# Kernel tuning notes

Hardware: AMD Instinct MI355X
Metric: run time of the kernel (lower is better)

Reference implementation:

```python
import jax, jax.numpy as jnp
import numpy as np

B, T, ND, SD, H = 4096, 256, 16, 8, 64
IN = SD + ND  # LSTM input dim


def setup_inputs() -> dict:
    key = jax.random.key(0)
    ks = jax.random.split(key, 20)
    def w(k, shape):
        fan_in = shape[0]
        return jax.random.normal(k, shape, jnp.float32) / np.sqrt(fan_in)
    return {
        "noise": jax.random.normal(ks[0], (B, T - 1, ND), jnp.float32),
        "eps": jax.random.normal(ks[1], (B, T - 1, SD), jnp.float32),
        "Wx": w(ks[2], (IN, 4 * H)),
        "Wh": w(ks[3], (H, 4 * H)),
        "b": jnp.zeros((4 * H,), jnp.float32),
        "Wm1": w(ks[4], (H, H)), "bm1": jnp.zeros((H,), jnp.float32),
        "Wm2": w(ks[5], (H, H)), "bm2": jnp.zeros((H,), jnp.float32),
        "Wm3": w(ks[6], (H, SD)), "bm3": jnp.zeros((SD,), jnp.float32),
        "Wv1": w(ks[7], (H, H)), "bv1": jnp.zeros((H,), jnp.float32),
        "Wv2": w(ks[8], (H, H)), "bv2": jnp.zeros((H,), jnp.float32),
        "Wv3": w(ks[9], (H, SD)), "bv3": jnp.zeros((SD,), jnp.float32),
    }


def reference(noise, eps, Wx, Wh, b, Wm1, bm1, Wm2, bm2, Wm3, bm3,
              Wv1, bv1, Wv2, bv2, Wv3, bv3):
    Bn = noise.shape[0]
    Hn = Wh.shape[0]
    Dn = Wm3.shape[1]

    def mlp(h, W1, b1, W2, b2, W3, b3):
        a = jax.nn.relu(h @ W1 + b1)
        a = jax.nn.relu(a @ W2 + b2)
        return a @ W3 + b3

    def step(carry, inp_t):
        x, h, c = carry
        n_t, e_t = inp_t
        # Keras LSTM: gates ordered i, f, g(cell), o
        z = jnp.concatenate([x, n_t], axis=-1) @ Wx + h @ Wh + b  # [B, 4H]
        i, f, g, o = jnp.split(z, 4, axis=-1)
        c = jax.nn.sigmoid(f) * c + jax.nn.sigmoid(i) * jnp.tanh(g)
        h = jax.nn.sigmoid(o) * jnp.tanh(c)
        mu = mlp(h, Wm1, bm1, Wm2, bm2, Wm3, bm3)
        std = jnp.exp(0.5 * mlp(h, Wv1, bv1, Wv2, bv2, Wv3, bv3))
        x = mu + std * e_t  # reparameterized Normal(mu, std).sample()
        return (x, h, c), x

    x0 = jnp.zeros((Bn, Dn), noise.dtype)  # log_series=True -> zeros
    h0 = jnp.zeros((Bn, Hn), noise.dtype)
    c0 = jnp.zeros((Bn, Hn), noise.dtype)
    noise_t = jnp.swapaxes(noise, 0, 1)  # [T-1, B, ND]
    eps_t = jnp.swapaxes(eps, 0, 1)      # [T-1, B, SD]
    _, xs = jax.lax.scan(step, (x0, h0, c0), (noise_t, eps_t))
    seq = jnp.concatenate([x0[:, None, :], jnp.swapaxes(xs, 0, 1)], axis=1)  # [B, T, SD]
    return jnp.cumsum(seq, axis=1)
```

## Files before the change

kernel.cpp:

```cpp
#include <hip/hip_runtime.h>

typedef _Float16 half8 __attribute__((ext_vector_type(8)));
typedef _Float16 half4 __attribute__((ext_vector_type(4)));
typedef float f32x4 __attribute__((ext_vector_type(4)));

#define TSTEPS 255
#define R 16
#define BLK 512
#define XSH 104
#define ZS 260
#define ASH 72

__device__ __forceinline__ float frcp(float x) { return __builtin_amdgcn_rcpf(x); }

__device__ __forceinline__ f32x4 mfma16(half8 a, half8 b, f32x4 c) {
  return __builtin_amdgcn_mfma_f32_16x16x32_f16(a, b, c, 0, 0, 0);
}

__global__ __launch_bounds__(BLK)
void genlstm_kernel(const float* __restrict__ noise,
                    const float* __restrict__ eps,
                    const float* __restrict__ Wx,
                    const float* __restrict__ Wh,
                    const float* __restrict__ bg,
                    const float* __restrict__ Wm1, const float* __restrict__ bm1,
                    const float* __restrict__ Wm2, const float* __restrict__ bm2,
                    const float* __restrict__ Wm3, const float* __restrict__ bm3,
                    const float* __restrict__ Wv1, const float* __restrict__ bv1,
                    const float* __restrict__ Wv2, const float* __restrict__ bv2,
                    const float* __restrict__ Wv3, const float* __restrict__ bv3,
                    float* __restrict__ out)
{
  __shared__ __align__(16) _Float16 xh[R][XSH];
  __shared__ __align__(16) _Float16 xl[R][XSH];
  __shared__ __align__(16) float    z2[R][ZS];
  __shared__ __align__(16) _Float16 a1h[2][R][ASH];
  __shared__ __align__(16) _Float16 a1l[2][R][ASH];
  __shared__ __align__(16) _Float16 a2h[2][R][ASH];
  __shared__ __align__(16) _Float16 a2l[2][R][ASH];
  __shared__ __align__(16) float    mulv[2][R][12];

  const int tid  = threadIdx.x;
  const int w    = tid >> 6;
  const int l    = tid & 63;
  const int lrow = l & 15;
  const int lq   = l >> 4;
  const long rowbase = (long)blockIdx.x * R;

  half8 gBhi[2][3], gBlo[2][3];
  #pragma unroll
  for (int t = 0; t < 2; ++t)
    #pragma unroll
    for (int kt = 0; kt < 3; ++kt)
      #pragma unroll
      for (int j = 0; j < 8; ++j) {
        int k  = 32 * kt + 8 * lq + j;
        int jc = 32 * w + 16 * t + lrow;
        int n  = 64 * (jc & 3) + (jc >> 2);
        float v = 0.f;
        if (k < 64) v = Wh[k * 256 + n];
        else if (k < 88) v = Wx[(k - 64) * 256 + n];
        _Float16 h = (_Float16)v;
        gBhi[t][kt][j] = h;
        gBlo[t][kt][j] = (_Float16)(v - (float)h);
      }

  const int chain = w >> 2;
  const int nt = w & 3;
  const float* W1 = chain ? Wv1 : Wm1;
  const float* W2 = chain ? Wv2 : Wm2;
  half8 B1hi[2], B1lo[2], B2hi[2], B2lo[2];
  #pragma unroll
  for (int kt = 0; kt < 2; ++kt)
    #pragma unroll
    for (int j = 0; j < 8; ++j) {
      int k = 32 * kt + 8 * lq + j;
      int n = 16 * nt + lrow;
      float v1 = W1[k * 64 + n];
      _Float16 h1 = (_Float16)v1;
      B1hi[kt][j] = h1; B1lo[kt][j] = (_Float16)(v1 - (float)h1);
      float v2 = W2[k * 64 + n];
      _Float16 h2 = (_Float16)v2;
      B2hi[kt][j] = h2; B2lo[kt][j] = (_Float16)(v2 - (float)h2);
    }

  half8 B3hi[2], B3lo[2];
  if (w < 2) {
    const float* W3 = w ? Wv3 : Wm3;
    #pragma unroll
    for (int kt = 0; kt < 2; ++kt)
      #pragma unroll
      for (int j = 0; j < 8; ++j) {
        int k = 32 * kt + 8 * lq + j;
        float v = (lrow < 8) ? W3[k * 8 + lrow] : 0.f;
        _Float16 h = (_Float16)v;
        B3hi[kt][j] = h;
        B3lo[kt][j] = (_Float16)(v - (float)h);
      }
  }

  const float bias1 = (chain ? bv1 : bm1)[16 * nt + lrow];
  const float bias2 = (chain ? bv2 : bm2)[16 * nt + lrow];
  float bias3 = 0.f;
  if (w < 2 && lrow < 8) bias3 = (w ? bv3 : bm3)[lrow];

  const float4 bgq = {bg[l], bg[64 + l], bg[128 + l], bg[192 + l]};

  float cst0 = 0.f, cst1 = 0.f;
  const int r5 = tid >> 3, d5 = tid & 7;
  float cum = 0.f;

  half8 hHi[2], hLo[2];
  #pragma unroll
  for (int kt = 0; kt < 2; ++kt)
    #pragma unroll
    for (int j = 0; j < 8; ++j) { hHi[kt][j] = (_Float16)0; hLo[kt][j] = (_Float16)0; }

  for (int i = tid; i < R * XSH; i += BLK) {
    (&xh[0][0])[i] = (_Float16)0;
    (&xl[0][0])[i] = (_Float16)0;
  }
  if (tid < 128) out[((rowbase + r5) * 256) * 8 + d5] = 0.f;
  __syncthreads();

  float4 nz = {0.f, 0.f, 0.f, 0.f};
  if (tid < 64) {
    int r = tid >> 2, j4 = (tid & 3) * 4;
    float4 n0 = *(const float4*)&noise[((rowbase + r) * TSTEPS) * 16 + j4];
    float tmp[4] = {n0.x, n0.y, n0.z, n0.w};
    half4 nh, nl;
    #pragma unroll
    for (int j = 0; j < 4; ++j) {
      _Float16 h = (_Float16)tmp[j];
      nh[j] = h; nl[j] = (_Float16)(tmp[j] - (float)h);
    }
    *(half4*)&xh[r][72 + j4] = nh;
    *(half4*)&xl[r][72 + j4] = nl;
    nz = *(const float4*)&noise[((rowbase + r) * TSTEPS + 1) * 16 + j4];
  }
  float ev = 0.f;
  if (tid < 128) ev = eps[((rowbase + r5) * TSTEPS) * 8 + d5];
  __syncthreads();

  for (int ts = 0; ts < TSTEPS; ++ts) {
    half8 Xhi = *(const half8*)&xh[lrow][64 + 8 * lq];
    half8 Xlo = *(const half8*)&xl[lrow][64 + 8 * lq];

    f32x4 accz0 = {0.f, 0.f, 0.f, 0.f};
    f32x4 accz1 = {0.f, 0.f, 0.f, 0.f};
    accz0 = mfma16(hHi[0], gBhi[0][0], accz0);
    accz1 = mfma16(hHi[0], gBhi[1][0], accz1);
    accz0 = mfma16(hLo[0], gBhi[0][0], accz0);
    accz1 = mfma16(hLo[0], gBhi[1][0], accz1);
    accz0 = mfma16(hHi[0], gBlo[0][0], accz0);
    accz1 = mfma16(hHi[0], gBlo[1][0], accz1);
    accz0 = mfma16(hHi[1], gBhi[0][1], accz0);
    accz1 = mfma16(hHi[1], gBhi[1][1], accz1);
    accz0 = mfma16(hLo[1], gBhi[0][1], accz0);
    accz1 = mfma16(hLo[1], gBhi[1][1], accz1);
    accz0 = mfma16(hHi[1], gBlo[0][1], accz0);
    accz1 = mfma16(hHi[1], gBlo[1][1], accz1);
    accz0 = mfma16(Xhi, gBhi[0][2], accz0);
    accz1 = mfma16(Xhi, gBhi[1][2], accz1);
    accz0 = mfma16(Xlo, gBhi[0][2], accz0);
    accz1 = mfma16(Xlo, gBhi[1][2], accz1);
    accz0 = mfma16(Xhi, gBlo[0][2], accz0);
    accz1 = mfma16(Xhi, gBlo[1][2], accz1);
    {
      const int r0 = 4 * lq;
      #pragma unroll
      for (int k = 0; k < 4; ++k) {
        z2[r0 + k][32 * w + lrow]      = accz0[k];
        z2[r0 + k][32 * w + 16 + lrow] = accz1[k];
      }
    }
    __syncthreads();

    #pragma unroll
    for (int rr = 0; rr < 2; ++rr) {
      const int r = w + rr * 8;
      float4 zq = *(const float4*)&z2[r][4 * l];
      float zi = zq.x + bgq.x;
      float zf = zq.y + bgq.y;
      float zg = zq.z + bgq.z;
      float zo = zq.w + bgq.w;
      float si = frcp(1.f + __expf(-zi));
      float sf = frcp(1.f + __expf(-zf));
      float so = frcp(1.f + __expf(-zo));
      float ag = fabsf(zg), eg = __expf(-2.f * ag);
      float tg = copysignf((1.f - eg) * frcp(1.f + eg), zg);
      float cs = rr ? cst1 : cst0;
      cs = fmaf(sf, cs, si * tg);
      if (rr) cst1 = cs; else cst0 = cs;
      float ac = fabsf(cs), ec = __expf(-2.f * ac);
      float tc = copysignf((1.f - ec) * frcp(1.f + ec), cs);
      float hv = so * tc;
      _Float16 hh = (_Float16)hv;
      xh[r][l] = hh;
      xl[r][l] = (_Float16)(hv - (float)hh);
    }
    if (tid < 64) {
      int r = tid >> 2, j4 = (tid & 3) * 4;
      float tmp[4] = {nz.x, nz.y, nz.z, nz.w};
      half4 nh, nl;
      #pragma unroll
      for (int j = 0; j < 4; ++j) {
        _Float16 h = (_Float16)tmp[j];
        nh[j] = h; nl[j] = (_Float16)(tmp[j] - (float)h);
      }
      *(half4*)&xh[r][72 + j4] = nh;
      *(half4*)&xl[r][72 + j4] = nl;
      if (ts + 2 < TSTEPS)
        nz = *(const float4*)&noise[((rowbase + r) * TSTEPS + ts + 2) * 16 + j4];
    }
    __syncthreads();

    {
      hHi[0] = *(const half8*)&xh[lrow][8 * lq];
      hHi[1] = *(const half8*)&xh[lrow][32 + 8 * lq];
      hLo[0] = *(const half8*)&xl[lrow][8 * lq];
      hLo[1] = *(const half8*)&xl[lrow][32 + 8 * lq];
      f32x4 acc = {0.f, 0.f, 0.f, 0.f};
      #pragma unroll
      for (int kt = 0; kt < 2; ++kt) {
        acc = mfma16(hHi[kt], B1hi[kt], acc);
        acc = mfma16(hLo[kt], B1hi[kt], acc);
        acc = mfma16(hHi[kt], B1lo[kt], acc);
      }
      const int r0 = 4 * lq;
      #pragma unroll
      for (int k = 0; k < 4; ++k) {
        float v = fmaxf(acc[k] + bias1, 0.f);
        _Float16 vh = (_Float16)v;
        a1h[chain][r0 + k][16 * nt + lrow] = vh;
        a1l[chain][r0 + k][16 * nt + lrow] = (_Float16)(v - (float)vh);
      }
    }
    __syncthreads();

    {
      half8 ahi0 = *(const half8*)&a1h[chain][lrow][8 * lq];
      half8 ahi1 = *(const half8*)&a1h[chain][lrow][32 + 8 * lq];
      half8 alo0 = *(const half8*)&a1l[chain][lrow][8 * lq];
      half8 alo1 = *(const half8*)&a1l[chain][lrow][32 + 8 * lq];
      f32x4 acc = {0.f, 0.f, 0.f, 0.f};
      acc = mfma16(ahi0, B2hi[0], acc);
      acc = mfma16(alo0, B2hi[0], acc);
      acc = mfma16(ahi0, B2lo[0], acc);
      acc = mfma16(ahi1, B2hi[1], acc);
      acc = mfma16(alo1, B2hi[1], acc);
      acc = mfma16(ahi1, B2lo[1], acc);
      const int r0 = 4 * lq;
      #pragma unroll
      for (int k = 0; k < 4; ++k) {
        float v = fmaxf(acc[k] + bias2, 0.f);
        _Float16 vh = (_Float16)v;
        a2h[chain][r0 + k][16 * nt + lrow] = vh;
        a2l[chain][r0 + k][16 * nt + lrow] = (_Float16)(v - (float)vh);
      }
    }
    __syncthreads();

    if (w < 2) {
      half8 chi0 = *(const half8*)&a2h[w][lrow][8 * lq];
      half8 chi1 = *(const half8*)&a2h[w][lrow][32 + 8 * lq];
      half8 clo0 = *(const half8*)&a2l[w][lrow][8 * lq];
      half8 clo1 = *(const half8*)&a2l[w][lrow][32 + 8 * lq];
      f32x4 acc = {0.f, 0.f, 0.f, 0.f};
      acc = mfma16(chi0, B3hi[0], acc);
      acc = mfma16(clo0, B3hi[0], acc);
      acc = mfma16(chi0, B3lo[0], acc);
      acc = mfma16(chi1, B3hi[1], acc);
      acc = mfma16(clo1, B3hi[1], acc);
      acc = mfma16(chi1, B3lo[1], acc);
      if (lrow < 8) {
        const int r0 = 4 * lq;
        #pragma unroll
        for (int k = 0; k < 4; ++k)
          mulv[w][r0 + k][lrow] = acc[k] + bias3;
      }
    }
    __syncthreads();

    if (tid < 128) {
      float mu = mulv[0][r5][d5];
      float lv = mulv[1][r5][d5];
      float x = fmaf(__expf(0.5f * lv), ev, mu);
      cum += x;
      out[((rowbase + r5) * 256 + ts + 1) * 8 + d5] = cum;
      _Float16 xhh = (_Float16)x;
      xh[r5][64 + d5] = xhh;
      xl[r5][64 + d5] = (_Float16)(x - (float)xhh);
      if (ts + 1 < TSTEPS)
        ev = eps[((rowbase + r5) * TSTEPS + ts + 1) * 8 + d5];
    }
    __syncthreads();
  }
}

extern "C" void kernel_launch(void* const* d_in, const int* in_sizes, int n_in,
                              void* d_out, int out_size, void* d_ws, size_t ws_size,
                              hipStream_t stream) {
  const float* noise = (const float*)d_in[0];
  const float* eps   = (const float*)d_in[1];
  const float* Wx    = (const float*)d_in[2];
  const float* Wh    = (const float*)d_in[3];
  const float* bg    = (const float*)d_in[4];
  const float* Wm1   = (const float*)d_in[5];
  const float* bm1   = (const float*)d_in[6];
  const float* Wm2   = (const float*)d_in[7];
  const float* bm2   = (const float*)d_in[8];
  const float* Wm3   = (const float*)d_in[9];
  const float* bm3   = (const float*)d_in[10];
  const float* Wv1   = (const float*)d_in[11];
  const float* bv1   = (const float*)d_in[12];
  const float* Wv2   = (const float*)d_in[13];
  const float* bv2   = (const float*)d_in[14];
  const float* Wv3   = (const float*)d_in[15];
  const float* bv3   = (const float*)d_in[16];
  float* out = (float*)d_out;

  dim3 grid(4096 / R), block(BLK);
  hipLaunchKernelGGL(genlstm_kernel, grid, block, 0, stream,
                     noise, eps, Wx, Wh, bg, Wm1, bm1, Wm2, bm2, Wm3, bm3,
                     Wv1, bv1, Wv2, bv2, Wv3, bv3, out);
}
```

Measured before the change: 589.1 us.

## Compute output head redundantly in every wave and pass x via shuffles, removing two barriers

Every wave now computes the final mu/logvar layer itself, in transposed form so that each lane holds four output dims for its batch row. The sampled x is packed as a hi/lo fp16 pair and handed to the next step's input operand through lane shuffles instead of shared memory. This removes the mulv shared buffer and two __syncthreads per timestep from a serial recurrence. In exchange, all eight waves repeat twelve MFMAs plus the exp and sample arithmetic each step, and the output store becomes a float4 from one wave.

```diff
diff --git a/kernel.cpp b/kernel.cpp
--- a/kernel.cpp
+++ b/kernel.cpp
@@ -2,6 +2,7 @@
 
 typedef _Float16 half8 __attribute__((ext_vector_type(8)));
 typedef _Float16 half4 __attribute__((ext_vector_type(4)));
+typedef unsigned short ushort8 __attribute__((ext_vector_type(8)));
 typedef float f32x4 __attribute__((ext_vector_type(4)));
 
 #define TSTEPS 255
@@ -15,6 +16,13 @@
 
 __device__ __forceinline__ f32x4 mfma16(half8 a, half8 b, f32x4 c) {
   return __builtin_amdgcn_mfma_f32_16x16x32_f16(a, b, c, 0, 0, 0);
+}
+
+__device__ __forceinline__ unsigned int packhl(float x) {
+  _Float16 hh = (_Float16)x;
+  _Float16 hl = (_Float16)(x - (float)hh);
+  return (unsigned int)__builtin_bit_cast(unsigned short, hh) |
+         ((unsigned int)__builtin_bit_cast(unsigned short, hl) << 16);
 }
 
 __global__ __launch_bounds__(BLK)
@@ -38,7 +46,6 @@
   __shared__ __align__(16) _Float16 a1l[2][R][ASH];
   __shared__ __align__(16) _Float16 a2h[2][R][ASH];
   __shared__ __align__(16) _Float16 a2l[2][R][ASH];
-  __shared__ __align__(16) float    mulv[2][R][12];
 
   const int tid  = threadIdx.x;
   const int w    = tid >> 6;
@@ -84,31 +91,34 @@
       B2hi[kt][j] = h2; B2lo[kt][j] = (_Float16)(v2 - (float)h2);
     }
 
-  half8 B3hi[2], B3lo[2];
-  if (w < 2) {
-    const float* W3 = w ? Wv3 : Wm3;
-    #pragma unroll
-    for (int kt = 0; kt < 2; ++kt)
-      #pragma unroll
-      for (int j = 0; j < 8; ++j) {
-        int k = 32 * kt + 8 * lq + j;
-        float v = (lrow < 8) ? W3[k * 8 + lrow] : 0.f;
-        _Float16 h = (_Float16)v;
-        B3hi[kt][j] = h;
-        B3lo[kt][j] = (_Float16)(v - (float)h);
-      }
-  }
+  half8 Amhi[2], Amlo[2], Avhi[2], Avlo[2];
+  #pragma unroll
+  for (int kt = 0; kt < 2; ++kt)
+    #pragma unroll
+    for (int j = 0; j < 8; ++j) {
+      int k = 32 * kt + 8 * lq + j;
+      float vm = (lrow < 8) ? Wm3[k * 8 + lrow] : 0.f;
+      _Float16 hm = (_Float16)vm;
+      Amhi[kt][j] = hm; Amlo[kt][j] = (_Float16)(vm - (float)hm);
+      float vv = (lrow < 8) ? Wv3[k * 8 + lrow] : 0.f;
+      _Float16 hv = (_Float16)vv;
+      Avhi[kt][j] = hv; Avlo[kt][j] = (_Float16)(vv - (float)hv);
+    }
 
   const float bias1 = (chain ? bv1 : bm1)[16 * nt + lrow];
   const float bias2 = (chain ? bv2 : bm2)[16 * nt + lrow];
-  float bias3 = 0.f;
-  if (w < 2 && lrow < 8) bias3 = (w ? bv3 : bm3)[lrow];
+
+  const int d0 = 4 * (lq & 1);
+  const float4 bm3q = *(const float4*)&bm3[d0];
+  const float4 bv3q = *(const float4*)&bv3[d0];
 
   const float4 bgq = {bg[l], bg[64 + l], bg[128 + l], bg[192 + l]};
 
   float cst0 = 0.f, cst1 = 0.f;
-  const int r5 = tid >> 3, d5 = tid & 7;
-  float cum = 0.f;
+
+  f32x4 cum4 = {0.f, 0.f, 0.f, 0.f};
+  float4 ep4 = {0.f, 0.f, 0.f, 0.f};
+  unsigned int pk0 = 0, pk1 = 0, pk2 = 0, pk3 = 0;
 
   half8 hHi[2], hLo[2];
   #pragma unroll
@@ -120,8 +130,10 @@
     (&xh[0][0])[i] = (_Float16)0;
     (&xl[0][0])[i] = (_Float16)0;
   }
-  if (tid < 128) out[((rowbase + r5) * 256) * 8 + d5] = 0.f;
-  __syncthreads();
+  {
+    const int r5 = tid >> 3, d5 = tid & 7;
+    if (tid < 128) out[((rowbase + r5) * 256) * 8 + d5] = 0.f;
+  }
 
   float4 nz = {0.f, 0.f, 0.f, 0.f};
   if (tid < 64) {
@@ -138,13 +150,31 @@
     *(half4*)&xl[r][72 + j4] = nl;
     nz = *(const float4*)&noise[((rowbase + r) * TSTEPS + 1) * 16 + j4];
   }
-  float ev = 0.f;
-  if (tid < 128) ev = eps[((rowbase + r5) * TSTEPS) * 8 + d5];
+  if (lq < 2) ep4 = *(const float4*)&eps[((rowbase + lrow) * TSTEPS) * 8 + d0];
   __syncthreads();
 
   for (int ts = 0; ts < TSTEPS; ++ts) {
     half8 Xhi = *(const half8*)&xh[lrow][64 + 8 * lq];
     half8 Xlo = *(const half8*)&xl[lrow][64 + 8 * lq];
+    {
+      unsigned int up0 = (unsigned int)__shfl_down((int)pk0, 16);
+      unsigned int up1 = (unsigned int)__shfl_down((int)pk1, 16);
+      unsigned int up2 = (unsigned int)__shfl_down((int)pk2, 16);
+      unsigned int up3 = (unsigned int)__shfl_down((int)pk3, 16);
+      if (lq == 0) {
+        ushort8 uh, ul;
+        uh[0] = (unsigned short)pk0; ul[0] = (unsigned short)(pk0 >> 16);
+        uh[1] = (unsigned short)pk1; ul[1] = (unsigned short)(pk1 >> 16);
+        uh[2] = (unsigned short)pk2; ul[2] = (unsigned short)(pk2 >> 16);
+        uh[3] = (unsigned short)pk3; ul[3] = (unsigned short)(pk3 >> 16);
+        uh[4] = (unsigned short)up0; ul[4] = (unsigned short)(up0 >> 16);
+        uh[5] = (unsigned short)up1; ul[5] = (unsigned short)(up1 >> 16);
+        uh[6] = (unsigned short)up2; ul[6] = (unsigned short)(up2 >> 16);
+        uh[7] = (unsigned short)up3; ul[7] = (unsigned short)(up3 >> 16);
+        Xhi = __builtin_bit_cast(half8, uh);
+        Xlo = __builtin_bit_cast(half8, ul);
+      }
+    }
 
     f32x4 accz0 = {0.f, 0.f, 0.f, 0.f};
     f32x4 accz1 = {0.f, 0.f, 0.f, 0.f};
@@ -261,40 +291,48 @@
     }
     __syncthreads();
 
-    if (w < 2) {
-      half8 chi0 = *(const half8*)&a2h[w][lrow][8 * lq];
-      half8 chi1 = *(const half8*)&a2h[w][lrow][32 + 8 * lq];
-      half8 clo0 = *(const half8*)&a2l[w][lrow][8 * lq];
-      half8 clo1 = *(const half8*)&a2l[w][lrow][32 + 8 * lq];
-      f32x4 acc = {0.f, 0.f, 0.f, 0.f};
-      acc = mfma16(chi0, B3hi[0], acc);
-      acc = mfma16(clo0, B3hi[0], acc);
-      acc = mfma16(chi0, B3lo[0], acc);
-      acc = mfma16(chi1, B3hi[1], acc);
-      acc = mfma16(clo1, B3hi[1], acc);
-      acc = mfma16(chi1, B3lo[1], acc);
-      if (lrow < 8) {
-        const int r0 = 4 * lq;
-        #pragma unroll
-        for (int k = 0; k < 4; ++k)
-          mulv[w][r0 + k][lrow] = acc[k] + bias3;
-      }
-    }
-    __syncthreads();
-
-    if (tid < 128) {
-      float mu = mulv[0][r5][d5];
-      float lv = mulv[1][r5][d5];
-      float x = fmaf(__expf(0.5f * lv), ev, mu);
-      cum += x;
-      out[((rowbase + r5) * 256 + ts + 1) * 8 + d5] = cum;
-      _Float16 xhh = (_Float16)x;
-      xh[r5][64 + d5] = xhh;
-      xl[r5][64 + d5] = (_Float16)(x - (float)xhh);
-      if (ts + 1 < TSTEPS)
-        ev = eps[((rowbase + r5) * TSTEPS + ts + 1) * 8 + d5];
-    }
-    __syncthreads();
+    f32x4 accm = {0.f, 0.f, 0.f, 0.f};
+    f32x4 accv = {0.f, 0.f, 0.f, 0.f};
+    {
+      half8 b0h0 = *(const half8*)&a2h[0][lrow][8 * lq];
+      half8 b0h1 = *(const half8*)&a2h[0][lrow][32 + 8 * lq];
+      half8 b0l0 = *(const half8*)&a2l[0][lrow][8 * lq];
+      half8 b0l1 = *(const half8*)&a2l[0][lrow][32 + 8 * lq];
+      accm = mfma16(Amhi[0], b0h0, accm);
+      accm = mfma16(Amlo[0], b0h0, accm);
+      accm = mfma16(Amhi[0], b0l0, accm);
+      accm = mfma16(Amhi[1], b0h1, accm);
+      accm = mfma16(Amlo[1], b0h1, accm);
+      accm = mfma16(Amhi[1], b0l1, accm);
+      half8 b1h0 = *(const half8*)&a2h[1][lrow][8 * lq];
+      half8 b1h1 = *(const half8*)&a2h[1][lrow][32 + 8 * lq];
+      half8 b1l0 = *(const half8*)&a2l[1][lrow][8 * lq];
+      half8 b1l1 = *(const half8*)&a2l[1][lrow][32 + 8 * lq];
+      accv = mfma16(Avhi[0], b1h0, accv);
+      accv = mfma16(Avlo[0], b1h0, accv);
+      accv = mfma16(Avhi[0], b1l0, accv);
+      accv = mfma16(Avhi[1], b1h1, accv);
+      accv = mfma16(Avlo[1], b1h1, accv);
+      accv = mfma16(Avhi[1], b1l1, accv);
+    }
+
+    {
+      float x0v = fmaf(__expf(0.5f * (accv[0] + bv3q.x)), ep4.x, accm[0] + bm3q.x);
+      float x1v = fmaf(__expf(0.5f * (accv[1] + bv3q.y)), ep4.y, accm[1] + bm3q.y);
+      float x2v = fmaf(__expf(0.5f * (accv[2] + bv3q.z)), ep4.z, accm[2] + bm3q.z);
+      float x3v = fmaf(__expf(0.5f * (accv[3] + bv3q.w)), ep4.w, accm[3] + bm3q.w);
+      cum4[0] += x0v; cum4[1] += x1v; cum4[2] += x2v; cum4[3] += x3v;
+      if (w == 0 && lq < 2) {
+        float4 cv = {cum4[0], cum4[1], cum4[2], cum4[3]};
+        *(float4*)&out[((rowbase + lrow) * 256 + ts + 1) * 8 + d0] = cv;
+      }
+      pk0 = packhl(x0v);
+      pk1 = packhl(x1v);
+      pk2 = packhl(x2v);
+      pk3 = packhl(x3v);
+      if (ts + 1 < TSTEPS && lq < 2)
+        ep4 = *(const float4*)&eps[((rowbase + lrow) * TSTEPS + ts + 1) * 8 + d0];
+    }
   }
 }
 
```

Result: slower. 626.2 us (+6.3%).
